# Performance work log

Measured on AMD Instinct MI355X. Metric: run time of the kernel, lower is better.

Reference implementation:

```python
import jax, jax.numpy as jnp
import numpy as np

# SMPL-style skeleton: parent index per joint (parent < child, root = -1)
PARENTS = [-1, 0, 0, 0, 1, 2, 3, 4, 5, 6, 7, 8, 9, 9, 9, 12, 13, 14, 16, 17, 18, 19, 20, 21]
END_SITES = [10, 11, 15, 22, 23]  # feet, head, hands
NUM_JOINTS = len(PARENTS)


def rot6d_to_matrix(x):
    """6D rotation rep -> 3x3 matrix via Gram-Schmidt. x: [..., 6] -> [..., 3, 3].
    eye(3).reshape(-1)[:6] = [1,0,0,0,1,0] maps to identity under this (row-stacked) convention."""
    a1, a2 = x[..., 0:3], x[..., 3:6]
    b1 = a1 / jnp.linalg.norm(a1, axis=-1, keepdims=True)
    a2p = a2 - jnp.sum(b1 * a2, axis=-1, keepdims=True) * b1
    b2 = a2p / jnp.linalg.norm(a2p, axis=-1, keepdims=True)
    b3 = jnp.cross(b1, b2)
    return jnp.stack([b1, b2, b3], axis=-2)


def fk_positions(rot, offsets):
    """Forward kinematics (faithful to _recompute_joint_global_info).
    rot: [F, J, 3, 3] local joint rotations; offsets: [F, J, 3].
    Returns global joint positions [F, J, 3]. Loop is over the fixed, small
    joint hierarchy (structural), fully vectorized over frames."""
    positions = [offsets[:, 0]]          # root: offset only
    orientations = [rot[:, 0]]           # root: local rotation
    for i in range(1, NUM_JOINTS):
        pi = PARENTS[i]
        po = orientations[pi]            # [F, 3, 3]
        pos = jnp.einsum('fab,fb->fa', po, offsets[:, i]) + positions[pi]
        positions.append(pos)
        orientations.append(po @ rot[:, i])
    return jnp.stack(positions, axis=1)  # [F, J, 3]


def setup_inputs() -> dict:
    key = jax.random.key(0)
    ks = jax.random.split(key, 6)
    F = 65536
    return {
        'poseA': jax.random.normal(ks[0], (F, NUM_JOINTS, 6), dtype=jnp.float32),
        'poseB': jax.random.normal(ks[1], (F, NUM_JOINTS, 6), dtype=jnp.float32),
        'joint_offsets_A': jax.random.normal(ks[2], (F, NUM_JOINTS, 3), dtype=jnp.float32),
        'joint_offsets_B': jax.random.normal(ks[3], (F, NUM_JOINTS, 3), dtype=jnp.float32),
        't_poseA': jax.random.normal(ks[4], (NUM_JOINTS, 3), dtype=jnp.float32),
        't_poseB': jax.random.normal(ks[5], (NUM_JOINTS, 3), dtype=jnp.float32),
    }


def reference(poseA, poseB, joint_offsets_A, joint_offsets_B, t_poseA, t_poseB):
    ee = jnp.array(END_SITES)
    # 6D -> rotation matrices (to_matrix)
    RA = rot6d_to_matrix(poseA)
    RB = rot6d_to_matrix(poseB)
    # sequential per-joint FK (the hot loop)
    posA = fk_positions(RA, joint_offsets_A)
    posB = fk_positions(RB, joint_offsets_B)
    # bbox scale from T-pose
    scale_A = jnp.max(t_poseA, axis=0) - jnp.min(t_poseA, axis=0)  # [3]
    scale_B = jnp.max(t_poseB, axis=0) - jnp.min(t_poseB, axis=0)
    eeA = posA[:, ee, :] - t_poseA[ee, :]   # [F, E, 3]
    eeB = posB[:, ee, :] - t_poseB[ee, :]
    loss = jnp.mean((eeA / scale_A - eeB / scale_B) ** 2)
    return loss
```

## Files before the change

kernel.cpp:

```cpp
#include <hip/hip_runtime.h>


struct V3 { float x, y, z; };
struct M3 { float m[3][3]; };

__device__ __forceinline__ V3 matvec(const M3& A, const V3& v) {
    return { A.m[0][0]*v.x + A.m[0][1]*v.y + A.m[0][2]*v.z,
             A.m[1][0]*v.x + A.m[1][1]*v.y + A.m[1][2]*v.z,
             A.m[2][0]*v.x + A.m[2][1]*v.y + A.m[2][2]*v.z };
}

__device__ __forceinline__ M3 matmul(const M3& A, const M3& B) {
    M3 C;
#pragma unroll
    for (int i = 0; i < 3; i++)
#pragma unroll
        for (int j = 0; j < 3; j++)
            C.m[i][j] = A.m[i][0]*B.m[0][j] + A.m[i][1]*B.m[1][j] + A.m[i][2]*B.m[2][j];
    return C;
}

template<int J>
__device__ __forceinline__ M3 rot6d_j(const float* __restrict__ frame) {
    const float* p = frame + 6 * J;
    float v0, v1, v2, v3, v4, v5;
    if constexpr ((J & 1) == 0) {
        float4 a = *(const float4*)p;
        float2 b = *(const float2*)(p + 4);
        v0 = a.x; v1 = a.y; v2 = a.z; v3 = a.w; v4 = b.x; v5 = b.y;
    } else {
        float2 a = *(const float2*)p;
        float4 b = *(const float4*)(p + 2);
        v0 = a.x; v1 = a.y; v2 = b.x; v3 = b.y; v4 = b.z; v5 = b.w;
    }
    float n1 = v0*v0 + v1*v1 + v2*v2;
    float r1 = 1.0f / sqrtf(n1);
    V3 b1 = { v0*r1, v1*r1, v2*r1 };
    float d = b1.x*v3 + b1.y*v4 + b1.z*v5;
    V3 u = { v3 - d*b1.x, v4 - d*b1.y, v5 - d*b1.z };
    float n2 = u.x*u.x + u.y*u.y + u.z*u.z;
    float r2 = 1.0f / sqrtf(n2);
    V3 b2 = { u.x*r2, u.y*r2, u.z*r2 };
    V3 b3 = { b1.y*b2.z - b1.z*b2.y, b1.z*b2.x - b1.x*b2.z, b1.x*b2.y - b1.y*b2.x };
    M3 R;
    R.m[0][0]=b1.x; R.m[0][1]=b1.y; R.m[0][2]=b1.z;
    R.m[1][0]=b2.x; R.m[1][1]=b2.y; R.m[1][2]=b2.z;
    R.m[2][0]=b3.x; R.m[2][1]=b3.y; R.m[2][2]=b3.z;
    return R;
}

template<int J>
__device__ __forceinline__ V3 load_off_j(const float* __restrict__ obase) {
    const float* p = obase + 3 * J;
    if constexpr ((J & 1) == 0) {
        float2 a = *(const float2*)p;
        float  b = p[2];
        return { a.x, a.y, b };
    } else {
        float  a = p[0];
        float2 b = *(const float2*)(p + 1);
        return { a, b.x, b.y };
    }
}

struct FK { M3 o; V3 p; };

template<int J>
__device__ __forceinline__ FK fk_step(const float* __restrict__ frame,
                                      const float* __restrict__ obase,
                                      const FK& par) {
    V3 off = load_off_j<J>(obase);
    V3 t = matvec(par.o, off);
    FK s;
    s.p = { par.p.x + t.x, par.p.y + t.y, par.p.z + t.z };
    s.o = matmul(par.o, rot6d_j<J>(frame));
    return s;
}

template<int J>
__device__ __forceinline__ V3 fk_end(const float* __restrict__ obase, const FK& par) {
    V3 off = load_off_j<J>(obase);
    V3 t = matvec(par.o, off);
    return { par.p.x + t.x, par.p.y + t.y, par.p.z + t.z };
}

__global__ __launch_bounds__(256, 4)
void ee_loss_kernel(const float* __restrict__ poseA, const float* __restrict__ poseB,
                    const float* __restrict__ offA,  const float* __restrict__ offB,
                    const float* __restrict__ tA,    const float* __restrict__ tB,
                    float* __restrict__ out, float inv_count) {
    const int tid  = threadIdx.x;
    const int wid  = tid >> 6;
    const int lane = tid & 63;
    const bool isB    = wid & 1;
    const bool isLong = wid & 2;
    const long long f = (long long)blockIdx.x * 64 + lane;

    const float* frame = (isB ? poseB : poseA) + f * 144;
    const float* obase = (isB ? offB  : offA ) + f * 72;

    __shared__ float s_eeB[64][15];
    __shared__ float s_inv[6];
    __shared__ float s_d[15];
    __shared__ float s_part[4];

    if (tid < 6) {
        const float* tp = (tid < 3) ? tA : tB;
        int ax = (tid < 3) ? tid : tid - 3;
        float mn = tp[ax], mx = mn;
#pragma unroll
        for (int j = 1; j < 24; j++) {
            float v = tp[j*3 + ax];
            mn = fminf(mn, v); mx = fmaxf(mx, v);
        }
        s_inv[tid] = 1.0f / (mx - mn);
    }
    if (tid < 15) {
        const int EE[5] = {10, 11, 15, 22, 23};
        int e = tid / 3, ax = tid - 3*e;
        int j = EE[e];
        float mnA = tA[ax], mxA = mnA, mnB = tB[ax], mxB = mnB;
#pragma unroll
        for (int k = 1; k < 24; k++) {
            float a = tA[k*3 + ax], b = tB[k*3 + ax];
            mnA = fminf(mnA, a); mxA = fmaxf(mxA, a);
            mnB = fminf(mnB, b); mxB = fmaxf(mxB, b);
        }
        s_d[tid] = tB[j*3 + ax]/(mxB - mnB) - tA[j*3 + ax]/(mxA - mnA);
    }

    float ee[9];
    int nee;
    if (!isLong) {
        FK r0; r0.o = rot6d_j<0>(frame); r0.p = load_off_j<0>(obase);
        FK a = fk_step<1>(frame, obase, r0);
        FK b = fk_step<2>(frame, obase, r0);
        a = fk_step<4>(frame, obase, a);
        b = fk_step<5>(frame, obase, b);
        a = fk_step<7>(frame, obase, a);
        b = fk_step<8>(frame, obase, b);
        V3 e10 = fk_end<10>(obase, a);
        V3 e11 = fk_end<11>(obase, b);
        ee[0]=e10.x; ee[1]=e10.y; ee[2]=e10.z;
        ee[3]=e11.x; ee[4]=e11.y; ee[5]=e11.z;
        nee = 6;
    } else {
        FK r0; r0.o = rot6d_j<0>(frame); r0.p = load_off_j<0>(obase);
        FK s = fk_step<3>(frame, obase, r0);
        s = fk_step<6>(frame, obase, s);
        s = fk_step<9>(frame, obase, s);
        FK sa = fk_step<12>(frame, obase, s);
        FK sb = fk_step<13>(frame, obase, s);
        FK sc = fk_step<14>(frame, obase, s);
        V3 e15 = fk_end<15>(obase, sa);
        sb = fk_step<16>(frame, obase, sb);
        sc = fk_step<17>(frame, obase, sc);
        sb = fk_step<18>(frame, obase, sb);
        sc = fk_step<19>(frame, obase, sc);
        sb = fk_step<20>(frame, obase, sb);
        sc = fk_step<21>(frame, obase, sc);
        V3 e22 = fk_end<22>(obase, sb);
        V3 e23 = fk_end<23>(obase, sc);
        ee[0]=e15.x; ee[1]=e15.y; ee[2]=e15.z;
        ee[3]=e22.x; ee[4]=e22.y; ee[5]=e22.z;
        ee[6]=e23.x; ee[7]=e23.y; ee[8]=e23.z;
        nee = 9;
    }

    const int base = isLong ? 6 : 0;
    if (isB) {
#pragma unroll 9
        for (int i = 0; i < 9; i++)
            if (i < nee) s_eeB[lane][base + i] = ee[i];
    }
    __syncthreads();

    float local = 0.0f;
    if (!isB) {
#pragma unroll 9
        for (int i = 0; i < 9; i++) {
            if (i < nee) {
                int col = base + i;
                int ax = col % 3;
                float t = ee[i]*s_inv[ax] - s_eeB[lane][col]*s_inv[3 + ax] + s_d[col];
                local += t * t;
            }
        }
        local *= inv_count;
    }
#pragma unroll
    for (int off = 32; off > 0; off >>= 1)
        local += __shfl_down(local, off, 64);
    if (lane == 0) s_part[wid] = local;
    __syncthreads();
    if (tid == 0) atomicAdd(out, (s_part[0] + s_part[1]) + (s_part[2] + s_part[3]));
}

extern "C" void kernel_launch(void* const* d_in, const int* in_sizes, int n_in,
                              void* d_out, int out_size, void* d_ws, size_t ws_size,
                              hipStream_t stream) {
    const float* poseA = (const float*)d_in[0];
    const float* poseB = (const float*)d_in[1];
    const float* offA  = (const float*)d_in[2];
    const float* offB  = (const float*)d_in[3];
    const float* tA    = (const float*)d_in[4];
    const float* tB    = (const float*)d_in[5];
    float* out = (float*)d_out;

    const int F = in_sizes[0] / 144;
    const int blocks = F / 64;
    const float inv_count = 1.0f / ((float)F * 15.0f);

    hipMemsetAsync(out, 0, sizeof(float), stream);
    ee_loss_kernel<<<blocks, 256, 0, stream>>>(poseA, poseB, offA, offB, tA, tB,
                                               out, inv_count);
}
```

Measured before the change: 175.0 us.

## Split FK work into one chain per end-effector across ten wavefronts

Instead of four wavefronts, where two handle the legs and two the spine plus arms, each block now runs ten wavefronts, one per end-effector chain per pose set. This shortens the longest serial dependency chain per wave and balances the work, which should raise parallelism and latency hiding. In exchange the shared root and spine joints (0, 3, 6, 9) are recomputed redundantly by several waves, adding ALU work and repeated loads. The branch is per-wave, so it does not cause divergence.

```diff
diff --git a/kernel.cpp b/kernel.cpp
--- a/kernel.cpp
+++ b/kernel.cpp
@@ -84,7 +84,7 @@
     return { par.p.x + t.x, par.p.y + t.y, par.p.z + t.z };
 }
 
-__global__ __launch_bounds__(256, 4)
+__global__ __launch_bounds__(640, 7)
 void ee_loss_kernel(const float* __restrict__ poseA, const float* __restrict__ poseB,
                     const float* __restrict__ offA,  const float* __restrict__ offB,
                     const float* __restrict__ tA,    const float* __restrict__ tB,
@@ -92,8 +92,8 @@
     const int tid  = threadIdx.x;
     const int wid  = tid >> 6;
     const int lane = tid & 63;
-    const bool isB    = wid & 1;
-    const bool isLong = wid & 2;
+    const int task = wid >> 1;
+    const bool isB = wid & 1;
     const long long f = (long long)blockIdx.x * 64 + lane;
 
     const float* frame = (isB ? poseB : poseA) + f * 144;
@@ -102,7 +102,7 @@
     __shared__ float s_eeB[64][15];
     __shared__ float s_inv[6];
     __shared__ float s_d[15];
-    __shared__ float s_part[4];
+    __shared__ float s_part[5];
 
     if (tid < 6) {
         const float* tp = (tid < 3) ? tA : tB;
@@ -129,71 +129,68 @@
         s_d[tid] = tB[j*3 + ax]/(mxB - mnB) - tA[j*3 + ax]/(mxA - mnA);
     }
 
-    float ee[9];
-    int nee;
-    if (!isLong) {
-        FK r0; r0.o = rot6d_j<0>(frame); r0.p = load_off_j<0>(obase);
-        FK a = fk_step<1>(frame, obase, r0);
-        FK b = fk_step<2>(frame, obase, r0);
-        a = fk_step<4>(frame, obase, a);
-        b = fk_step<5>(frame, obase, b);
-        a = fk_step<7>(frame, obase, a);
-        b = fk_step<8>(frame, obase, b);
-        V3 e10 = fk_end<10>(obase, a);
-        V3 e11 = fk_end<11>(obase, b);
-        ee[0]=e10.x; ee[1]=e10.y; ee[2]=e10.z;
-        ee[3]=e11.x; ee[4]=e11.y; ee[5]=e11.z;
-        nee = 6;
-    } else {
-        FK r0; r0.o = rot6d_j<0>(frame); r0.p = load_off_j<0>(obase);
-        FK s = fk_step<3>(frame, obase, r0);
-        s = fk_step<6>(frame, obase, s);
-        s = fk_step<9>(frame, obase, s);
-        FK sa = fk_step<12>(frame, obase, s);
-        FK sb = fk_step<13>(frame, obase, s);
-        FK sc = fk_step<14>(frame, obase, s);
-        V3 e15 = fk_end<15>(obase, sa);
-        sb = fk_step<16>(frame, obase, sb);
-        sc = fk_step<17>(frame, obase, sc);
-        sb = fk_step<18>(frame, obase, sb);
-        sc = fk_step<19>(frame, obase, sc);
-        sb = fk_step<20>(frame, obase, sb);
-        sc = fk_step<21>(frame, obase, sc);
-        V3 e22 = fk_end<22>(obase, sb);
-        V3 e23 = fk_end<23>(obase, sc);
-        ee[0]=e15.x; ee[1]=e15.y; ee[2]=e15.z;
-        ee[3]=e22.x; ee[4]=e22.y; ee[5]=e22.z;
-        ee[6]=e23.x; ee[7]=e23.y; ee[8]=e23.z;
-        nee = 9;
-    }
-
-    const int base = isLong ? 6 : 0;
+    V3 e;
+    {
+        FK s; s.o = rot6d_j<0>(frame); s.p = load_off_j<0>(obase);
+        if (task == 0) {
+            s = fk_step<1>(frame, obase, s);
+            s = fk_step<4>(frame, obase, s);
+            s = fk_step<7>(frame, obase, s);
+            e = fk_end<10>(obase, s);
+        } else if (task == 1) {
+            s = fk_step<2>(frame, obase, s);
+            s = fk_step<5>(frame, obase, s);
+            s = fk_step<8>(frame, obase, s);
+            e = fk_end<11>(obase, s);
+        } else if (task == 2) {
+            s = fk_step<3>(frame, obase, s);
+            s = fk_step<6>(frame, obase, s);
+            s = fk_step<9>(frame, obase, s);
+            s = fk_step<12>(frame, obase, s);
+            e = fk_end<15>(obase, s);
+        } else if (task == 3) {
+            s = fk_step<3>(frame, obase, s);
+            s = fk_step<6>(frame, obase, s);
+            s = fk_step<9>(frame, obase, s);
+            s = fk_step<13>(frame, obase, s);
+            s = fk_step<16>(frame, obase, s);
+            s = fk_step<18>(frame, obase, s);
+            s = fk_step<20>(frame, obase, s);
+            e = fk_end<22>(obase, s);
+        } else {
+            s = fk_step<3>(frame, obase, s);
+            s = fk_step<6>(frame, obase, s);
+            s = fk_step<9>(frame, obase, s);
+            s = fk_step<14>(frame, obase, s);
+            s = fk_step<17>(frame, obase, s);
+            s = fk_step<19>(frame, obase, s);
+            s = fk_step<21>(frame, obase, s);
+            e = fk_end<23>(obase, s);
+        }
+    }
+
+    const int col0 = task * 3;
     if (isB) {
-#pragma unroll 9
-        for (int i = 0; i < 9; i++)
-            if (i < nee) s_eeB[lane][base + i] = ee[i];
+        s_eeB[lane][col0 + 0] = e.x;
+        s_eeB[lane][col0 + 1] = e.y;
+        s_eeB[lane][col0 + 2] = e.z;
     }
     __syncthreads();
 
     float local = 0.0f;
     if (!isB) {
-#pragma unroll 9
-        for (int i = 0; i < 9; i++) {
-            if (i < nee) {
-                int col = base + i;
-                int ax = col % 3;
-                float t = ee[i]*s_inv[ax] - s_eeB[lane][col]*s_inv[3 + ax] + s_d[col];
-                local += t * t;
-            }
-        }
-        local *= inv_count;
-    }
-#pragma unroll
-    for (int off = 32; off > 0; off >>= 1)
-        local += __shfl_down(local, off, 64);
-    if (lane == 0) s_part[wid] = local;
+        float tx = e.x*s_inv[0] - s_eeB[lane][col0 + 0]*s_inv[3] + s_d[col0 + 0];
+        float ty = e.y*s_inv[1] - s_eeB[lane][col0 + 1]*s_inv[4] + s_d[col0 + 1];
+        float tz = e.z*s_inv[2] - s_eeB[lane][col0 + 2]*s_inv[5] + s_d[col0 + 2];
+        local = (tx*tx + ty*ty + tz*tz) * inv_count;
+#pragma unroll
+        for (int off = 32; off > 0; off >>= 1)
+            local += __shfl_down(local, off, 64);
+        if (lane == 0) s_part[task] = local;
+    }
     __syncthreads();
-    if (tid == 0) atomicAdd(out, (s_part[0] + s_part[1]) + (s_part[2] + s_part[3]));
+    if (tid == 0)
+        atomicAdd(out, ((s_part[0] + s_part[1]) + (s_part[2] + s_part[3])) + s_part[4]);
 }
 
 extern "C" void kernel_launch(void* const* d_in, const int* in_sizes, int n_in,
@@ -212,6 +209,6 @@
     const float inv_count = 1.0f / ((float)F * 15.0f);
 
     hipMemsetAsync(out, 0, sizeof(float), stream);
-    ee_loss_kernel<<<blocks, 256, 0, stream>>>(poseA, poseB, offA, offB, tA, tB,
+    ee_loss_kernel<<<blocks, 640, 0, stream>>>(poseA, poseB, offA, offB, tA, tB,
                                                out, inv_count);
 }
```

Result: slower. 217.2 us (+24.1%).

## Stage pose and offset data through LDS with coalesced loads, one frame per thread

Applied to the files above, without the earlier changes.

Replaces strided per-thread global loads of pose and offset data (each thread reading its own 576-byte frame) with cooperative, coalesced loads into padded shared-memory tiles. The skeleton is processed in four joint-range stages separated by barriers. Each thread now computes the full 24-joint FK for one frame instead of splitting short and long chains across waves, and each block handles 128 frames. The goal is better global-memory coalescing. The cost is roughly 57KB of LDS per block, extra barriers, a lower occupancy target, and a longer serial chain per thread.

```diff
diff --git a/kernel.cpp b/kernel.cpp
--- a/kernel.cpp
+++ b/kernel.cpp
@@ -20,19 +20,14 @@
     return C;
 }
 
-template<int J>
-__device__ __forceinline__ M3 rot6d_j(const float* __restrict__ frame) {
-    const float* p = frame + 6 * J;
-    float v0, v1, v2, v3, v4, v5;
-    if constexpr ((J & 1) == 0) {
-        float4 a = *(const float4*)p;
-        float2 b = *(const float2*)(p + 4);
-        v0 = a.x; v1 = a.y; v2 = a.z; v3 = a.w; v4 = b.x; v5 = b.y;
-    } else {
-        float2 a = *(const float2*)p;
-        float4 b = *(const float4*)(p + 2);
-        v0 = a.x; v1 = a.y; v2 = b.x; v3 = b.y; v4 = b.z; v5 = b.w;
-    }
+#define PPAD 37
+#define OPAD 19
+
+struct FK { M3 o; V3 p; };
+
+__device__ __forceinline__ M3 rot6d_lds(const float* __restrict__ sp, int base) {
+    float v0 = sp[base+0], v1 = sp[base+1], v2 = sp[base+2];
+    float v3 = sp[base+3], v4 = sp[base+4], v5 = sp[base+5];
     float n1 = v0*v0 + v1*v1 + v2*v2;
     float r1 = 1.0f / sqrtf(n1);
     V3 b1 = { v0*r1, v1*r1, v2*r1 };
@@ -49,60 +44,46 @@
     return R;
 }
 
-template<int J>
-__device__ __forceinline__ V3 load_off_j(const float* __restrict__ obase) {
-    const float* p = obase + 3 * J;
-    if constexpr ((J & 1) == 0) {
-        float2 a = *(const float2*)p;
-        float  b = p[2];
-        return { a.x, a.y, b };
-    } else {
-        float  a = p[0];
-        float2 b = *(const float2*)(p + 1);
-        return { a, b.x, b.y };
-    }
-}
-
-struct FK { M3 o; V3 p; };
-
-template<int J>
-__device__ __forceinline__ FK fk_step(const float* __restrict__ frame,
-                                      const float* __restrict__ obase,
-                                      const FK& par) {
-    V3 off = load_off_j<J>(obase);
+__device__ __forceinline__ FK fk_step_l(const float* __restrict__ sp,
+                                        const float* __restrict__ so,
+                                        int pbase, int obase, const FK& par) {
+    V3 off = { so[obase], so[obase+1], so[obase+2] };
     V3 t = matvec(par.o, off);
     FK s;
     s.p = { par.p.x + t.x, par.p.y + t.y, par.p.z + t.z };
-    s.o = matmul(par.o, rot6d_j<J>(frame));
+    s.o = matmul(par.o, rot6d_lds(sp, pbase));
     return s;
 }
 
-template<int J>
-__device__ __forceinline__ V3 fk_end(const float* __restrict__ obase, const FK& par) {
-    V3 off = load_off_j<J>(obase);
+__device__ __forceinline__ V3 fk_end_l(const float* __restrict__ so,
+                                       int obase, const FK& par) {
+    V3 off = { so[obase], so[obase+1], so[obase+2] };
     V3 t = matvec(par.o, off);
     return { par.p.x + t.x, par.p.y + t.y, par.p.z + t.z };
 }
 
-__global__ __launch_bounds__(256, 4)
+__global__ __launch_bounds__(256)
+__attribute__((amdgpu_waves_per_eu(2)))
 void ee_loss_kernel(const float* __restrict__ poseA, const float* __restrict__ poseB,
                     const float* __restrict__ offA,  const float* __restrict__ offB,
                     const float* __restrict__ tA,    const float* __restrict__ tB,
                     float* __restrict__ out, float inv_count) {
-    const int tid  = threadIdx.x;
-    const int wid  = tid >> 6;
-    const int lane = tid & 63;
-    const bool isB    = wid & 1;
-    const bool isLong = wid & 2;
-    const long long f = (long long)blockIdx.x * 64 + lane;
-
-    const float* frame = (isB ? poseB : poseA) + f * 144;
-    const float* obase = (isB ? offB  : offA ) + f * 72;
-
-    __shared__ float s_eeB[64][15];
+    __shared__ float s_pose[256 * PPAD];
+    __shared__ float s_off [256 * OPAD];
+    __shared__ float s_eeB[128][15];
     __shared__ float s_inv[6];
     __shared__ float s_d[15];
-    __shared__ float s_part[4];
+    __shared__ float s_part[2];
+
+    const int tid = threadIdx.x;
+    const int fl  = tid & 127;
+    const bool isB = tid >= 128;
+    const int f0w_p = blockIdx.x * 128 * 144;
+    const int f0w_o = blockIdx.x * 128 * 72;
+    const float* pA = poseA + f0w_p;
+    const float* pB = poseB + f0w_p;
+    const float* oA = offA  + f0w_o;
+    const float* oB = offB  + f0w_o;
 
     if (tid < 6) {
         const float* tp = (tid < 3) ? tA : tB;
@@ -129,71 +110,105 @@
         s_d[tid] = tB[j*3 + ax]/(mxB - mnB) - tA[j*3 + ax]/(mxA - mnA);
     }
 
-    float ee[9];
-    int nee;
-    if (!isLong) {
-        FK r0; r0.o = rot6d_j<0>(frame); r0.p = load_off_j<0>(obase);
-        FK a = fk_step<1>(frame, obase, r0);
-        FK b = fk_step<2>(frame, obase, r0);
-        a = fk_step<4>(frame, obase, a);
-        b = fk_step<5>(frame, obase, b);
-        a = fk_step<7>(frame, obase, a);
-        b = fk_step<8>(frame, obase, b);
-        V3 e10 = fk_end<10>(obase, a);
-        V3 e11 = fk_end<11>(obase, b);
-        ee[0]=e10.x; ee[1]=e10.y; ee[2]=e10.z;
-        ee[3]=e11.x; ee[4]=e11.y; ee[5]=e11.z;
-        nee = 6;
-    } else {
-        FK r0; r0.o = rot6d_j<0>(frame); r0.p = load_off_j<0>(obase);
-        FK s = fk_step<3>(frame, obase, r0);
-        s = fk_step<6>(frame, obase, s);
-        s = fk_step<9>(frame, obase, s);
-        FK sa = fk_step<12>(frame, obase, s);
-        FK sb = fk_step<13>(frame, obase, s);
-        FK sc = fk_step<14>(frame, obase, s);
-        V3 e15 = fk_end<15>(obase, sa);
-        sb = fk_step<16>(frame, obase, sb);
-        sc = fk_step<17>(frame, obase, sc);
-        sb = fk_step<18>(frame, obase, sb);
-        sc = fk_step<19>(frame, obase, sc);
-        sb = fk_step<20>(frame, obase, sb);
-        sc = fk_step<21>(frame, obase, sc);
-        V3 e22 = fk_end<22>(obase, sb);
-        V3 e23 = fk_end<23>(obase, sc);
-        ee[0]=e15.x; ee[1]=e15.y; ee[2]=e15.z;
-        ee[3]=e22.x; ee[4]=e22.y; ee[5]=e22.z;
-        ee[6]=e23.x; ee[7]=e23.y; ee[8]=e23.z;
-        nee = 9;
-    }
-
-    const int base = isLong ? 6 : 0;
+    auto stage = [&](int st) {
+        const int ps = st * 36, os = st * 18;
+#pragma unroll
+        for (int k = 0; k < 18; k++) {
+            int i = tid + k * 256;
+            int flr = i / 36, w = i - flr * 36;
+            s_pose[flr * PPAD + w] = pA[flr * 144 + ps + w];
+        }
+#pragma unroll
+        for (int k = 0; k < 18; k++) {
+            int i = tid + k * 256;
+            int flr = i / 36, w = i - flr * 36;
+            s_pose[(128 + flr) * PPAD + w] = pB[flr * 144 + ps + w];
+        }
+#pragma unroll
+        for (int k = 0; k < 9; k++) {
+            int i = tid + k * 256;
+            int flr = i / 18, w = i - flr * 18;
+            s_off[flr * OPAD + w] = oA[flr * 72 + os + w];
+        }
+#pragma unroll
+        for (int k = 0; k < 9; k++) {
+            int i = tid + k * 256;
+            int flr = i / 18, w = i - flr * 18;
+            s_off[(128 + flr) * OPAD + w] = oB[flr * 72 + os + w];
+        }
+    };
+
+    const float* sp = s_pose + tid * PPAD;
+    const float* so = s_off  + tid * OPAD;
+
+    stage(0);
+    __syncthreads();
+    FK s0; s0.o = rot6d_lds(sp, 0); s0.p = { so[0], so[1], so[2] };
+    FK s1 = fk_step_l(sp, so,  6,  3, s0);
+    FK s2 = fk_step_l(sp, so, 12,  6, s0);
+    FK s3 = fk_step_l(sp, so, 18,  9, s0);
+    FK s4 = fk_step_l(sp, so, 24, 12, s1);
+    FK s5 = fk_step_l(sp, so, 30, 15, s2);
+    __syncthreads();
+
+    stage(1);
+    __syncthreads();
+    FK s6 = fk_step_l(sp, so,  0,  0, s3);
+    FK s7 = fk_step_l(sp, so,  6,  3, s4);
+    FK s8 = fk_step_l(sp, so, 12,  6, s5);
+    FK s9 = fk_step_l(sp, so, 18,  9, s6);
+    V3 e10 = fk_end_l(so, 12, s7);
+    V3 e11 = fk_end_l(so, 15, s8);
+    __syncthreads();
+
+    stage(2);
+    __syncthreads();
+    FK s12 = fk_step_l(sp, so,  0,  0, s9);
+    FK s13 = fk_step_l(sp, so,  6,  3, s9);
+    FK s14 = fk_step_l(sp, so, 12,  6, s9);
+    V3 e15 = fk_end_l(so, 9, s12);
+    FK s16 = fk_step_l(sp, so, 24, 12, s13);
+    FK s17 = fk_step_l(sp, so, 30, 15, s14);
+    __syncthreads();
+
+    stage(3);
+    __syncthreads();
+    FK s18 = fk_step_l(sp, so,  0,  0, s16);
+    FK s19 = fk_step_l(sp, so,  6,  3, s17);
+    FK s20 = fk_step_l(sp, so, 12,  6, s18);
+    FK s21 = fk_step_l(sp, so, 18,  9, s19);
+    V3 e22 = fk_end_l(so, 12, s20);
+    V3 e23 = fk_end_l(so, 15, s21);
+    __syncthreads();
+
     if (isB) {
-#pragma unroll 9
-        for (int i = 0; i < 9; i++)
-            if (i < nee) s_eeB[lane][base + i] = ee[i];
+        s_eeB[fl][ 0] = e10.x; s_eeB[fl][ 1] = e10.y; s_eeB[fl][ 2] = e10.z;
+        s_eeB[fl][ 3] = e11.x; s_eeB[fl][ 4] = e11.y; s_eeB[fl][ 5] = e11.z;
+        s_eeB[fl][ 6] = e15.x; s_eeB[fl][ 7] = e15.y; s_eeB[fl][ 8] = e15.z;
+        s_eeB[fl][ 9] = e22.x; s_eeB[fl][10] = e22.y; s_eeB[fl][11] = e22.z;
+        s_eeB[fl][12] = e23.x; s_eeB[fl][13] = e23.y; s_eeB[fl][14] = e23.z;
     }
     __syncthreads();
 
     float local = 0.0f;
     if (!isB) {
-#pragma unroll 9
-        for (int i = 0; i < 9; i++) {
-            if (i < nee) {
-                int col = base + i;
-                int ax = col % 3;
-                float t = ee[i]*s_inv[ax] - s_eeB[lane][col]*s_inv[3 + ax] + s_d[col];
-                local += t * t;
-            }
+        float eeA[15] = { e10.x, e10.y, e10.z, e11.x, e11.y, e11.z,
+                          e15.x, e15.y, e15.z, e22.x, e22.y, e22.z,
+                          e23.x, e23.y, e23.z };
+#pragma unroll
+        for (int i = 0; i < 15; i++) {
+            int ax = i % 3;
+            float t = eeA[i]*s_inv[ax] - s_eeB[fl][i]*s_inv[3 + ax] + s_d[i];
+            local += t * t;
         }
         local *= inv_count;
-    }
-#pragma unroll
-    for (int off = 32; off > 0; off >>= 1)
-        local += __shfl_down(local, off, 64);
-    if (lane == 0) s_part[wid] = local;
-    __syncthreads();
-    if (tid == 0) atomicAdd(out, (s_part[0] + s_part[1]) + (s_part[2] + s_part[3]));
+#pragma unroll
+        for (int off = 32; off > 0; off >>= 1)
+            local += __shfl_down(local, off, 64);
+        if ((tid & 63) == 0) s_part[tid >> 6] = local;
+    }
+    __syncthreads();
+    if (tid == 0) atomicAdd(out, s_part[0] + s_part[1]);
 }
 
 extern "C" void kernel_launch(void* const* d_in, const int* in_sizes, int n_in,
@@ -208,7 +223,7 @@
     float* out = (float*)d_out;
 
     const int F = in_sizes[0] / 144;
-    const int blocks = F / 64;
+    const int blocks = F / 128;
     const float inv_count = 1.0f / ((float)F * 15.0f);
 
     hipMemsetAsync(out, 0, sizeof(float), stream);
```

After: 222.8 us. +27.3%, slower.
